# Performance work log

Measured on AMD Instinct MI355X. Metric: run time of the kernel, lower is better.

Reference implementation:

```python
import jax, jax.numpy as jnp
import numpy as np
import math

# dims
B, L, D = 2, 2048, 1024          # batch, seq len, embedding_dim
HID, ATT, H = 1024, 512, 8       # linear_hidden_dim, attention_dim, num_heads
DQK, DUV = ATT // H, HID // H    # 64, 128
NBUCK = 64                       # time_num_buckets
MAX_SPAN = 86400 * 90            # max_time_span
EPS = 1e-6
OUT_DIM = 2 * HID + 2 * ATT      # uvqk output dim = 3072


def _time_boundaries():
    # RelativeAttentionBiasModule._build_boundaries: pure log buckets
    steps = NBUCK - 1
    log_part = np.exp(np.linspace(0.0, math.log(MAX_SPAN), steps))
    b = np.unique(np.floor(np.clip(log_part, 1, None)).astype(np.int64)).astype(np.float32)
    return jnp.asarray(b)

_BOUNDARIES = _time_boundaries()  # len <= 63, indices < NBUCK


def setup_inputs() -> dict:
    key = jax.random.key(0)
    ks = jax.random.split(key, 8)
    x = jax.random.normal(ks[0], (B, L, D), dtype=jnp.float32)
    timestamps = jnp.sort(
        jax.random.randint(ks[1], (B, L), 0, 2592000), axis=-1
    )  # chronological event times (seconds)
    attn_mask = jnp.tril(jnp.ones((L, L), dtype=bool))[None].repeat(B, axis=0)  # causal
    W_uvqk = jax.random.normal(ks[2], (OUT_DIM, D), dtype=jnp.float32) * 0.02
    b_uvqk = jnp.zeros((OUT_DIM,), dtype=jnp.float32)
    time_bias = jax.random.normal(ks[3], (NBUCK, H), dtype=jnp.float32) * 0.02
    W_o = jax.random.normal(ks[4], (D, HID), dtype=jnp.float32) * 0.02
    b_o = jnp.zeros((D,), dtype=jnp.float32)
    rms_w = jnp.ones((HID,), dtype=jnp.float32)
    return {"x": x, "timestamps": timestamps, "attn_mask": attn_mask,
            "W_uvqk": W_uvqk, "b_uvqk": b_uvqk, "time_bias": time_bias,
            "W_o": W_o, "b_o": b_o, "rms_w": rms_w}


def reference(x, timestamps, attn_mask, W_uvqk, b_uvqk, time_bias, W_o, b_o, rms_w):
    Bx, Lx, _ = x.shape
    scale = 1.0 / math.sqrt(DQK)

    # fused uvqk projection + act1 (silu)
    h = jax.nn.silu(x @ W_uvqk.T + b_uvqk)  # [B, L, OUT_DIM]
    u, v, q, k = jnp.split(h, [HID, 2 * HID, 2 * HID + ATT], axis=-1)

    def heads(t, d):  # [B, L, H*d] -> [B, H, L, d]
        return t.reshape(Bx, Lx, H, d).transpose(0, 2, 1, 3)

    u = heads(u, DUV)
    v = heads(v, DUV)
    q = heads(q, DQK) * scale
    k = heads(k, DQK)

    logits = jnp.einsum('bhid,bhjd->bhij', q.astype(jnp.float32), k.astype(jnp.float32))

    # bucketized relative-time bias (per-head)
    tdiff = jnp.abs(timestamps[:, :, None] - timestamps[:, None, :])
    tdiff = jnp.clip(tdiff, 1, None).astype(jnp.float32)  # clamp_min(1)
    bk = jnp.searchsorted(_BOUNDARIES, tdiff, side='left')  # torch.bucketize right=False
    rab = time_bias[bk].transpose(0, 3, 1, 2)  # [B, H, L, L]

    # pointwise silu attention (no softmax), masked
    A = jax.nn.silu(logits + rab) * attn_mask[:, None].astype(jnp.float32)

    y = jnp.einsum('bhij,bhjd->bhid', A, v)               # [B, H, L, DUV]
    y = y.transpose(0, 2, 1, 3).reshape(Bx, Lx, HID)       # merge heads
    u_m = u.transpose(0, 2, 1, 3).reshape(Bx, Lx, HID)

    # RMSNorm then U-gate
    rms = y * jax.lax.rsqrt(jnp.mean(y * y, axis=-1, keepdims=True) + EPS) * rms_w
    y_point = rms.astype(x.dtype) * u_m

    return y_point @ W_o.T + b_o  # [B, L, D]
```

## Files before the change

kernel.cpp:

```cpp
#include <hip/hip_runtime.h>
#include <hip/hip_bf16.h>

typedef float f32x4 __attribute__((ext_vector_type(4)));
typedef short s16x8 __attribute__((ext_vector_type(8)));
typedef short s16x4 __attribute__((ext_vector_type(4)));
typedef unsigned short u16x4 __attribute__((ext_vector_type(4)));

__device__ __forceinline__ float bf2f(unsigned short u) {
    union { unsigned int i; float f; } x; x.i = ((unsigned int)u) << 16; return x.f;
}
__device__ __forceinline__ unsigned short f2bf(float f) {
    union { float f; unsigned int i; } x; x.f = f;
    unsigned int r = x.i + 0x7FFFu + ((x.i >> 16) & 1u);
    return (unsigned short)(r >> 16);
}
__device__ __forceinline__ float silu_fast(float v) {
    return v * __builtin_amdgcn_rcpf(1.f + __expf(-v));
}

#define GLDS16(gp, lp) __builtin_amdgcn_global_load_lds( \
    (const __attribute__((address_space(1))) unsigned int*)(gp), \
    (__attribute__((address_space(3))) unsigned int*)(lp), 16, 0, 0)

__global__ __launch_bounds__(256) void cvt_bucketize(
    const float* __restrict__ X, const float* __restrict__ W,
    const float* __restrict__ Wo, const int* __restrict__ TS,
    unsigned short* __restrict__ Xb, unsigned short* __restrict__ Wb,
    unsigned short* __restrict__ Wob, unsigned char* __restrict__ BK)
{
    const int tid = threadIdx.x;
    if (blockIdx.x < 8192) {
        int idx = blockIdx.x * 256 + tid;
        const float* src; unsigned short* dst; int off;
        if (idx < 1048576)       { src = X;  dst = Xb;  off = idx; }
        else if (idx < 1835008)  { src = W;  dst = Wb;  off = idx - 1048576; }
        else                     { src = Wo; dst = Wob; off = idx - 1835008; }
        f32x4 v = *reinterpret_cast<const f32x4*>(&src[(size_t)off * 4]);
        u16x4 o;
        #pragma unroll
        for (int j = 0; j < 4; ++j) o[j] = f2bf(v[j]);
        *reinterpret_cast<u16x4*>(&dst[(size_t)off * 4]) = o;
        return;
    }
    const int bid = blockIdx.x - 8192;
    const int jt = bid & 31, it = (bid >> 5) & 31, b = bid >> 10;
    if (jt > it) return;
    __shared__ int bndRaw[63];
    __shared__ int bnd[64];
    __shared__ int tsi[64], tsj[64];
    if (tid < 63) {
        double step = log(7776000.0) / 62.0;
        double v = exp(step * (double)tid);
        if (v < 1.0) v = 1.0;
        bndRaw[tid] = (int)floor(v);
    }
    if (tid >= 64 && tid < 128) tsi[tid - 64] = TS[b * 2048 + it * 64 + (tid - 64)];
    else if (tid >= 128 && tid < 192) tsj[tid - 128] = TS[b * 2048 + jt * 64 + (tid - 128)];
    __syncthreads();
    if (tid == 0) {
        int c = 0, p = -1;
        for (int i = 0; i < 63; ++i) { int x = bndRaw[i]; if (x != p) { bnd[c++] = x; p = x; } }
        for (; c < 64; ++c) bnd[c] = 0x7FFFFFFF;
    }
    __syncthreads();
    const int il = tid & 63, jc = (tid >> 6) * 16;
    const int tiv = tsi[il];
    unsigned char out[16];
    #pragma unroll
    for (int u = 0; u < 16; ++u) {
        int td = tiv - tsj[jc + u]; td = td < 0 ? -td : td; if (td < 1) td = 1;
        int pos = 0;
        #pragma unroll
        for (int st = 32; st; st >>= 1)
            if (bnd[pos + st - 1] < td) pos += st;
        out[u] = (unsigned char)pos;
    }
    *reinterpret_cast<int4*>(&BK[((size_t)b << 22) + (size_t)(it * 64 + il) * 2048 + jt * 64 + jc]) =
        *reinterpret_cast<const int4*>(out);
}

__global__ __launch_bounds__(256) void gemm_uvqk(
    const unsigned short* __restrict__ Xb, const unsigned short* __restrict__ Wb,
    const float* __restrict__ bias,
    unsigned short* __restrict__ U, unsigned short* __restrict__ Vt,
    unsigned short* __restrict__ Q, unsigned short* __restrict__ K)
{
    __shared__ __align__(16) unsigned short sA[128][64];
    __shared__ __align__(16) unsigned short sB[128][64];
    const int tid = threadIdx.x;
    const int wv = tid >> 6, lane = tid & 63;
    const int g = lane >> 4, lr = lane & 15;
    const int wid = (blockIdx.x & 7) * 96 + (blockIdx.x >> 3);
    const int m0 = (wid & 31) * 128, n0 = (wid >> 5) * 128;
    const int wr = (wv >> 1) * 64, wc = (wv & 1) * 64;
    const int ls = lr & 7;
    f32x4 acc[4][4] = {};

    for (int k0 = 0; k0 < 1024; k0 += 64) {
        #pragma unroll
        for (int c = 0; c < 4; ++c) {
            int id = c * 256 + tid;
            int row = id >> 3, c8 = id & 7;
            int sc = (c8 ^ (row & 7)) * 8;
            GLDS16(&Xb[(size_t)(m0 + row) * 1024 + k0 + sc], &sA[row][c8 * 8]);
            GLDS16(&Wb[(size_t)(n0 + row) * 1024 + k0 + sc], &sB[row][c8 * 8]);
        }
        __syncthreads();
        #pragma unroll
        for (int kq = 0; kq < 2; ++kq) {
            s16x8 afr[4], bfr[4];
            #pragma unroll
            for (int i = 0; i < 4; ++i) {
                afr[i] = *reinterpret_cast<const s16x8*>(
                    &sA[wr + i * 16 + lr][((kq * 4 + g) ^ ls) * 8]);
                bfr[i] = *reinterpret_cast<const s16x8*>(
                    &sB[wc + i * 16 + lr][((kq * 4 + g) ^ ls) * 8]);
            }
            #pragma unroll
            for (int mi = 0; mi < 4; ++mi)
                #pragma unroll
                for (int ni = 0; ni < 4; ++ni)
                    acc[mi][ni] = __builtin_amdgcn_mfma_f32_16x16x32_bf16(
                        afr[mi], bfr[ni], acc[mi][ni], 0, 0, 0);
        }
        __syncthreads();
    }

    if (n0 >= 1024 && n0 < 2048) {
        const int head = (n0 - 1024) >> 7;
        unsigned short* sT = &sA[0][0] + wv * (32 * 72);
        #pragma unroll
        for (int hh = 0; hh < 2; ++hh) {
            #pragma unroll
            for (int nn = 0; nn < 2; ++nn) {
                int ni = hh * 2 + nn;
                float bn = bias[n0 + wc + ni * 16 + lr];
                #pragma unroll
                for (int mi = 0; mi < 4; ++mi)
                    #pragma unroll
                    for (int r = 0; r < 4; ++r)
                        sT[(nn * 16 + lr) * 72 + mi * 16 + g * 4 + r] =
                            f2bf(silu_fast(acc[mi][ni][r] + bn));
            }
            #pragma unroll
            for (int c = 0; c < 4; ++c) {
                int id = c * 64 + lane;
                int row = id >> 3, ch = id & 7;
                s16x8 val = *reinterpret_cast<const s16x8*>(&sT[row * 72 + ch * 8]);
                int d = wc + hh * 32 + row;
                int mg = m0 + wr + ch * 8;
                int bb = mg >> 11, l = mg & 2047;
                *reinterpret_cast<s16x8*>(
                    &Vt[(((size_t)(bb * 8 + head) * 128 + d) << 11) + l]) = val;
            }
        }
    } else {
        #pragma unroll
        for (int ni = 0; ni < 4; ++ni) {
            int n = n0 + wc + ni * 16 + lr;
            float bn = bias[n];
            #pragma unroll
            for (int mi = 0; mi < 4; ++mi) {
                #pragma unroll
                for (int r = 0; r < 4; ++r) {
                    int m = m0 + wr + mi * 16 + g * 4 + r;
                    float v = silu_fast(acc[mi][ni][r] + bn);
                    int b = m >> 11, l = m & 2047;
                    if (n < 1024) {
                        U[(size_t)m * 1024 + n] = f2bf(v);
                    } else if (n < 2560) {
                        int dd = n - 2048, h = dd >> 6, d = dd & 63;
                        Q[((((size_t)(b * 8 + h) << 11) + l) << 6) + d] = f2bf(v * 0.125f);
                    } else {
                        int dd = n - 2560, h = dd >> 6, d = dd & 63;
                        K[((((size_t)(b * 8 + h) << 11) + l) << 6) + d] = f2bf(v);
                    }
                }
            }
        }
    }
}

__global__ __launch_bounds__(512, 1) void attn(
    const unsigned short* __restrict__ Q, const unsigned short* __restrict__ K,
    const unsigned short* __restrict__ Vt, const unsigned char* __restrict__ BK,
    const float* __restrict__ TB, unsigned short* __restrict__ Y)
{
    __shared__ __align__(16) unsigned short sK[2][2][64][64];
    __shared__ __align__(16) unsigned short sV[2][2][128][64];
    __shared__ __align__(16) unsigned char  sBK[2][2][64][64];

    const int tid = threadIdx.x, wv = tid >> 6, lane = tid & 63;
    const int g = lane >> 4, lr = lane & 15;

    const int bid = blockIdx.x;
    const int xcd = bid & 7, kix = bid >> 3;
    const int bh = 2 * xcd + (kix & 1);
    const int ti = 31 - (kix >> 1);
    const int b = bh >> 3, h = bh & 7;
    const int i0 = ti * 64;
    const int rg = wv & 3;
    const int half = wv >> 2;
    const int irow = i0 + rg * 16;
    const int P = (ti + 2) >> 1;

    const int tbl = __float_as_int(TB[lane * 8 + h]);

    const unsigned short* qb = Q + ((size_t)bh << 11) * 64;
    const unsigned short* kb = K + ((size_t)bh << 11) * 64;
    const unsigned short* vtb = Vt + ((size_t)bh << 7) * 2048;
    const unsigned char* bkb = BK + ((size_t)b << 22);

    s16x8 aq[2];
    #pragma unroll
    for (int kq = 0; kq < 2; ++kq)
        aq[kq] = *reinterpret_cast<const s16x8*>(&qb[(size_t)(irow + lr) * 64 + kq * 32 + g * 8]);

    char* sKb = (char*)&sK[0][0][0][0];
    char* sVb = (char*)&sV[0][0][0][0];
    char* sBKb = (char*)&sBK[0][0][0][0];
    const int cs = lr & 7;
    const int ib = irow + lr;

    auto stage = [&](int q, int db) {
        int jth = 2 * q + half;
        if (jth > ti) jth = 2 * q;
        const size_t j0 = (size_t)jth * 64;
        char* kd = sKb + db * 16384 + half * 8192;
        char* vd = sVb + db * 32768 + half * 16384;
        char* bkd = sBKb + db * 8192 + half * 4096;
        #pragma unroll
        for (int c = 0; c < 2; ++c) {
            int chunk = rg * 128 + c * 64 + lane;
            int row = chunk >> 3, c8 = chunk & 7;
            GLDS16(kb + (j0 + row) * 64 + ((c8 ^ (row & 7)) * 8), kd + chunk * 16);
        }
        #pragma unroll
        for (int c = 0; c < 4; ++c) {
            int chunk = rg * 256 + c * 64 + lane;
            int d = chunk >> 3, c8 = chunk & 7;
            GLDS16(vtb + (size_t)d * 2048 + j0 + ((c8 ^ (d & 7)) * 8), vd + chunk * 16);
        }
        {
            int chunk = rg * 64 + lane;
            int row = chunk >> 2, c16 = chunk & 3;
            GLDS16(bkb + (size_t)(i0 + row) * 2048 + j0 + ((c16 ^ (row & 3)) * 16), bkd + chunk * 16);
        }
    };

    f32x4 accy[8] = {};

#define COMPUTE(DB) { \
        const int jt = 2 * p + half; \
        if (jt <= ti) { \
            const char* kbase = sKb + (DB) * 16384 + half * 8192; \
            f32x4 sacc[4] = {}; \
            _Pragma("unroll") \
            for (int ni = 0; ni < 4; ++ni) { \
                _Pragma("unroll") \
                for (int kq = 0; kq < 2; ++kq) { \
                    s16x8 kf = *reinterpret_cast<const s16x8*>( \
                        kbase + (ni * 16 + lr) * 128 + (((kq * 4 + g) ^ cs) << 4)); \
                    sacc[ni] = __builtin_amdgcn_mfma_f32_16x16x32_bf16(kf, aq[kq], sacc[ni], 0, 0, 0); \
                } \
            } \
            const int j0 = jt * 64; \
            const bool diag = (jt == ti); \
            s16x4 pf[4]; \
            _Pragma("unroll") \
            for (int ni = 0; ni < 4; ++ni) { \
                unsigned int bw = *reinterpret_cast<const unsigned int*>( \
                    sBKb + (DB) * 8192 + half * 4096 + (rg * 16 + lr) * 64 + ((ni ^ (lr & 3)) << 4) + g * 4); \
                float b0 = __int_as_float(__builtin_amdgcn_ds_bpermute((int)((bw & 255u) << 2), tbl)); \
                float b1 = __int_as_float(__builtin_amdgcn_ds_bpermute((int)(((bw >> 8) & 255u) << 2), tbl)); \
                float b2 = __int_as_float(__builtin_amdgcn_ds_bpermute((int)(((bw >> 16) & 255u) << 2), tbl)); \
                float b3 = __int_as_float(__builtin_amdgcn_ds_bpermute((int)((bw >> 24) << 2), tbl)); \
                float v0 = silu_fast(sacc[ni][0] + b0); \
                float v1 = silu_fast(sacc[ni][1] + b1); \
                float v2 = silu_fast(sacc[ni][2] + b2); \
                float v3 = silu_fast(sacc[ni][3] + b3); \
                if (diag) { \
                    int jb = j0 + ni * 16 + g * 4; \
                    if (jb + 0 > ib) v0 = 0.f; \
                    if (jb + 1 > ib) v1 = 0.f; \
                    if (jb + 2 > ib) v2 = 0.f; \
                    if (jb + 3 > ib) v3 = 0.f; \
                } \
                unsigned int w0, w1; \
                asm("v_cvt_pk_bf16_f32 %0, %1, %2" : "=v"(w0) : "v"(v0), "v"(v1)); \
                asm("v_cvt_pk_bf16_f32 %0, %1, %2" : "=v"(w1) : "v"(v2), "v"(v3)); \
                union { unsigned int u_[2]; s16x4 v_; } cvt_; \
                cvt_.u_[0] = w0; cvt_.u_[1] = w1; \
                pf[ni] = cvt_.v_; \
            } \
            const char* vbase = sVb + (DB) * 32768 + half * 16384; \
            _Pragma("unroll") \
            for (int di = 0; di < 8; ++di) { \
                _Pragma("unroll") \
                for (int ni = 0; ni < 4; ++ni) { \
                    s16x4 vf = *reinterpret_cast<const s16x4*>( \
                        vbase + (di * 16 + lr) * 128 + (((2 * ni + (g >> 1)) ^ cs) << 4) + ((g & 1) << 3)); \
                    accy[di] = __builtin_amdgcn_mfma_f32_16x16x16bf16_1k(pf[ni], vf, accy[di], 0, 0, 0); \
                } \
            } \
        } }

    stage(0, 0);

    int p = 0;
    for (;;) {
        __builtin_amdgcn_s_barrier();
        if (p + 1 < P) {
            stage(p + 1, 1);
            asm volatile("s_waitcnt vmcnt(7)" ::: "memory");
        } else {
            asm volatile("s_waitcnt vmcnt(0)" ::: "memory");
        }
        __builtin_amdgcn_s_barrier();
        COMPUTE(0);
        if (++p == P) break;
        __builtin_amdgcn_s_barrier();
        if (p + 1 < P) {
            stage(p + 1, 0);
            asm volatile("s_waitcnt vmcnt(7)" ::: "memory");
        } else {
            asm volatile("s_waitcnt vmcnt(0)" ::: "memory");
        }
        __builtin_amdgcn_s_barrier();
        COMPUTE(1);
        if (++p == P) break;
    }
#undef COMPUTE

    __syncthreads();
    float* red = (float*)sVb;
    if (wv >= 4) {
        #pragma unroll
        for (int di = 0; di < 8; ++di)
            #pragma unroll
            for (int r = 0; r < 4; ++r)
                red[(rg * 16 + g * 4 + r) * 132 + di * 16 + lr] = accy[di][r];
    }
    __syncthreads();
    if (wv < 4) {
        #pragma unroll
        for (int di = 0; di < 8; ++di)
            #pragma unroll
            for (int r = 0; r < 4; ++r) {
                float s = accy[di][r] + red[(rg * 16 + g * 4 + r) * 132 + di * 16 + lr];
                Y[(size_t)((b << 11) + irow + g * 4 + r) * 1024 + h * 128 + di * 16 + lr] = f2bf(s);
            }
    }
}

__global__ __launch_bounds__(256) void rmsnorm_gate(
    const unsigned short* __restrict__ Y, const unsigned short* __restrict__ U,
    const float* __restrict__ rw, unsigned short* __restrict__ YP)
{
    __shared__ float red[4];
    const int row = blockIdx.x, tid = threadIdx.x;
    u16x4 v4 = *reinterpret_cast<const u16x4*>(&Y[(size_t)row * 1024 + tid * 4]);
    float v[4];
    #pragma unroll
    for (int j = 0; j < 4; ++j) v[j] = bf2f(v4[j]);
    float ss = v[0] * v[0] + v[1] * v[1] + v[2] * v[2] + v[3] * v[3];
    #pragma unroll
    for (int off = 32; off; off >>= 1) ss += __shfl_down(ss, off);
    if ((tid & 63) == 0) red[tid >> 6] = ss;
    __syncthreads();
    float rms = rsqrtf((red[0] + red[1] + red[2] + red[3]) * (1.f / 1024.f) + 1e-6f);
    #pragma unroll
    for (int j = 0; j < 4; ++j) {
        int c = tid * 4 + j;
        float o = v[j] * rms * rw[c] * bf2f(U[(size_t)row * 1024 + c]);
        YP[(size_t)row * 1024 + c] = f2bf(o);
    }
}

__global__ __launch_bounds__(512) void gemm_out(
    const unsigned short* __restrict__ YP, const unsigned short* __restrict__ Wob,
    const float* __restrict__ bo, float* __restrict__ OUT)
{
    __shared__ __align__(16) unsigned short sA[128][64];
    __shared__ __align__(16) unsigned short sB[128][64];
    const int tid = threadIdx.x;
    const int wv = tid >> 6, lane = tid & 63;
    const int g = lane >> 4, lr = lane & 15;
    const int wid = (blockIdx.x & 7) * 32 + (blockIdx.x >> 3);
    const int m0 = (wid & 31) * 128, n0 = (wid >> 5) * 128;
    const int wr = (wv >> 2) * 64, wc = (wv & 3) * 32;
    const int ls = lr & 7;
    f32x4 acc[4][2] = {};

    for (int k0 = 0; k0 < 1024; k0 += 64) {
        #pragma unroll
        for (int c = 0; c < 2; ++c) {
            int id = c * 512 + tid;
            int row = id >> 3, c8 = id & 7;
            int sc = (c8 ^ (row & 7)) * 8;
            GLDS16(&YP[(size_t)(m0 + row) * 1024 + k0 + sc], &sA[row][c8 * 8]);
            GLDS16(&Wob[(size_t)(n0 + row) * 1024 + k0 + sc], &sB[row][c8 * 8]);
        }
        __syncthreads();
        #pragma unroll
        for (int kq = 0; kq < 2; ++kq) {
            s16x8 afr[4], bfr[2];
            #pragma unroll
            for (int i = 0; i < 4; ++i)
                afr[i] = *reinterpret_cast<const s16x8*>(
                    &sA[wr + i * 16 + lr][((kq * 4 + g) ^ ls) * 8]);
            #pragma unroll
            for (int i = 0; i < 2; ++i)
                bfr[i] = *reinterpret_cast<const s16x8*>(
                    &sB[wc + i * 16 + lr][((kq * 4 + g) ^ ls) * 8]);
            #pragma unroll
            for (int mi = 0; mi < 4; ++mi)
                #pragma unroll
                for (int ni = 0; ni < 2; ++ni)
                    acc[mi][ni] = __builtin_amdgcn_mfma_f32_16x16x32_bf16(
                        afr[mi], bfr[ni], acc[mi][ni], 0, 0, 0);
        }
        __syncthreads();
    }

    #pragma unroll
    for (int ni = 0; ni < 2; ++ni) {
        int n = n0 + wc + ni * 16 + lr;
        float bn = bo[n];
        #pragma unroll
        for (int mi = 0; mi < 4; ++mi)
            #pragma unroll
            for (int r = 0; r < 4; ++r) {
                int m = m0 + wr + mi * 16 + g * 4 + r;
                OUT[(size_t)m * 1024 + n] = acc[mi][ni][r] + bn;
            }
    }
}

extern "C" void kernel_launch(void* const* d_in, const int* in_sizes, int n_in,
                              void* d_out, int out_size, void* d_ws, size_t ws_size,
                              hipStream_t stream) {
    const float* X     = (const float*)d_in[0];
    const int*   TS    = (const int*)d_in[1];
    const float* Wuvqk = (const float*)d_in[3];
    const float* buvqk = (const float*)d_in[4];
    const float* TB    = (const float*)d_in[5];
    const float* Wo    = (const float*)d_in[6];
    const float* bo    = (const float*)d_in[7];
    const float* rw    = (const float*)d_in[8];
    float* OUT = (float*)d_out;

    char* ws = (char*)d_ws;
    unsigned short* Qb  = (unsigned short*)(ws);
    unsigned short* Kb  = (unsigned short*)(ws + (4u << 20));
    unsigned short* Vt  = (unsigned short*)(ws + (8u << 20));
    unsigned short* Ub  = (unsigned short*)(ws + (16u << 20));
    unsigned short* Yb  = (unsigned short*)(ws + (24u << 20));
    unsigned short* Xb  = (unsigned short*)(ws + (24u << 20));
    unsigned short* Wb  = (unsigned short*)(ws + (32u << 20));
    unsigned short* YP  = (unsigned short*)(ws + (40u << 20));
    unsigned char*  BKm = (unsigned char*)(ws + (48u << 20));
    unsigned short* Wob = (unsigned short*)(ws + (56u << 20));

    cvt_bucketize<<<10240, 256, 0, stream>>>(X, Wuvqk, Wo, TS, Xb, Wb, Wob, BKm);
    gemm_uvqk<<<768, 256, 0, stream>>>(Xb, Wb, buvqk, Ub, Vt, Qb, Kb);
    attn<<<512, 512, 0, stream>>>(Qb, Kb, Vt, BKm, TB, Yb);
    rmsnorm_gate<<<4096, 256, 0, stream>>>(Yb, Ub, rw, YP);
    gemm_out<<<256, 512, 0, stream>>>(YP, Wob, bo, OUT);
}
```

Measured before the change: 144.6 us.

## Shrink attention KV tile to 32 columns and load bias bytes directly to registers

The attention kernel now stages 32-column K/V tiles per half-block instead of 64, which halves shared memory to 48KB and raises the launch-bounds occupancy hint from 1 to 6. The diagonal masking is simplified to the last iteration. Time-bucket indices are loaded from global memory straight into registers one stage ahead, instead of going through LDS. The aim is more resident blocks and less LDS traffic, at the cost of twice as many pipeline steps with their barriers and smaller MFMA batches. The raised occupancy hint may also squeeze the register budget.

Measured after the change: 174.9 us. 1.21x slower.

```diff
diff --git a/kernel.cpp b/kernel.cpp
--- a/kernel.cpp
+++ b/kernel.cpp
@@ -181,14 +181,12 @@
     }
 }
 
-__global__ __launch_bounds__(512, 1) void attn(
+__global__ __launch_bounds__(512, 6) void attn(
     const unsigned short* __restrict__ Q, const unsigned short* __restrict__ K,
     const unsigned short* __restrict__ Vt, const unsigned char* __restrict__ BK,
     const float* __restrict__ TB, unsigned short* __restrict__ Y)
 {
-    __shared__ __align__(16) unsigned short sK[2][2][64][64];
-    __shared__ __align__(16) unsigned short sV[2][2][128][64];
-    __shared__ __align__(16) unsigned char  sBK[2][2][64][64];
+    __shared__ __align__(16) char smem[49152];
 
     const int tid = threadIdx.x, wv = tid >> 6, lane = tid & 63;
     const int g = lane >> 4, lr = lane & 15;
@@ -202,138 +200,133 @@
     const int rg = wv & 3;
     const int half = wv >> 2;
     const int irow = i0 + rg * 16;
-    const int P = (ti + 2) >> 1;
+    const int P = ti + 1;
 
     const int tbl = __float_as_int(TB[lane * 8 + h]);
 
     const unsigned short* qb = Q + ((size_t)bh << 11) * 64;
     const unsigned short* kb = K + ((size_t)bh << 11) * 64;
     const unsigned short* vtb = Vt + ((size_t)bh << 7) * 2048;
-    const unsigned char* bkb = BK + ((size_t)b << 22);
+    const unsigned char* bkp = BK + ((size_t)b << 22) + (size_t)(irow + lr) * 2048 + g * 4;
 
     s16x8 aq[2];
     #pragma unroll
     for (int kq = 0; kq < 2; ++kq)
         aq[kq] = *reinterpret_cast<const s16x8*>(&qb[(size_t)(irow + lr) * 64 + kq * 32 + g * 8]);
 
-    char* sKb = (char*)&sK[0][0][0][0];
-    char* sVb = (char*)&sV[0][0][0][0];
-    char* sBKb = (char*)&sBK[0][0][0][0];
+    char* base = smem;
     const int cs = lr & 7;
     const int ib = irow + lr;
 
-    auto stage = [&](int q, int db) {
-        int jth = 2 * q + half;
-        if (jth > ti) jth = 2 * q;
-        const size_t j0 = (size_t)jth * 64;
-        char* kd = sKb + db * 16384 + half * 8192;
-        char* vd = sVb + db * 32768 + half * 16384;
-        char* bkd = sBKb + db * 8192 + half * 4096;
+    auto stage = [&](int p, int db) {
+        const int jt = 2 * p + half;
+        const size_t j0 = (size_t)jt * 32;
+        char* kd = base + db * 8192 + half * 4096;
+        char* vd = base + 16384 + db * 16384 + half * 8192;
+        {
+            int id = (rg << 6) | lane;
+            int row = id >> 3, c8 = id & 7;
+            GLDS16(kb + (j0 + row) * 64 + ((c8 ^ (row & 7)) * 8), kd + id * 16);
+        }
         #pragma unroll
         for (int c = 0; c < 2; ++c) {
-            int chunk = rg * 128 + c * 64 + lane;
-            int row = chunk >> 3, c8 = chunk & 7;
-            GLDS16(kb + (j0 + row) * 64 + ((c8 ^ (row & 7)) * 8), kd + chunk * 16);
-        }
-        #pragma unroll
-        for (int c = 0; c < 4; ++c) {
-            int chunk = rg * 256 + c * 64 + lane;
-            int d = chunk >> 3, c8 = chunk & 7;
-            GLDS16(vtb + (size_t)d * 2048 + j0 + ((c8 ^ (d & 7)) * 8), vd + chunk * 16);
-        }
-        {
-            int chunk = rg * 64 + lane;
-            int row = chunk >> 2, c16 = chunk & 3;
-            GLDS16(bkb + (size_t)(i0 + row) * 2048 + j0 + ((c16 ^ (row & 3)) * 16), bkd + chunk * 16);
+            int id = c * 256 + ((rg << 6) | lane);
+            int d = id >> 2, c16 = id & 3;
+            GLDS16(vtb + (size_t)d * 2048 + j0 + ((c16 ^ (d & 3)) * 8), vd + id * 16);
         }
     };
 
+#define BIAS_LOAD(p, bw) { const unsigned char* p_ = bkp + (size_t)(2 * (p) + half) * 32; \
+        bw[0] = *(const unsigned int*)(p_); bw[1] = *(const unsigned int*)(p_ + 16); }
+
     f32x4 accy[8] = {};
 
-#define COMPUTE(DB) { \
-        const int jt = 2 * p + half; \
-        if (jt <= ti) { \
-            const char* kbase = sKb + (DB) * 16384 + half * 8192; \
-            f32x4 sacc[4] = {}; \
+#define COMPUTE(DB, BW, p) { \
+        const int jt = 2 * (p) + half; \
+        const char* kbase = base + (DB) * 8192 + half * 4096; \
+        f32x4 sacc[2] = {}; \
+        _Pragma("unroll") \
+        for (int ni = 0; ni < 2; ++ni) { \
             _Pragma("unroll") \
-            for (int ni = 0; ni < 4; ++ni) { \
-                _Pragma("unroll") \
-                for (int kq = 0; kq < 2; ++kq) { \
-                    s16x8 kf = *reinterpret_cast<const s16x8*>( \
-                        kbase + (ni * 16 + lr) * 128 + (((kq * 4 + g) ^ cs) << 4)); \
-                    sacc[ni] = __builtin_amdgcn_mfma_f32_16x16x32_bf16(kf, aq[kq], sacc[ni], 0, 0, 0); \
-                } \
+            for (int kq = 0; kq < 2; ++kq) { \
+                s16x8 kf = *reinterpret_cast<const s16x8*>( \
+                    kbase + (ni * 16 + lr) * 128 + (((kq * 4 + g) ^ cs) << 4)); \
+                sacc[ni] = __builtin_amdgcn_mfma_f32_16x16x32_bf16(kf, aq[kq], sacc[ni], 0, 0, 0); \
             } \
-            const int j0 = jt * 64; \
-            const bool diag = (jt == ti); \
-            s16x4 pf[4]; \
+        } \
+        const int j0 = jt * 32; \
+        const bool diag = ((p) == P - 1); \
+        s16x4 pf[2]; \
+        _Pragma("unroll") \
+        for (int ni = 0; ni < 2; ++ni) { \
+            unsigned int bw = BW[ni]; \
+            float b0 = __int_as_float(__builtin_amdgcn_ds_bpermute((int)((bw & 255u) << 2), tbl)); \
+            float b1 = __int_as_float(__builtin_amdgcn_ds_bpermute((int)(((bw >> 8) & 255u) << 2), tbl)); \
+            float b2 = __int_as_float(__builtin_amdgcn_ds_bpermute((int)(((bw >> 16) & 255u) << 2), tbl)); \
+            float b3 = __int_as_float(__builtin_amdgcn_ds_bpermute((int)((bw >> 24) << 2), tbl)); \
+            float v0 = silu_fast(sacc[ni][0] + b0); \
+            float v1 = silu_fast(sacc[ni][1] + b1); \
+            float v2 = silu_fast(sacc[ni][2] + b2); \
+            float v3 = silu_fast(sacc[ni][3] + b3); \
+            if (diag) { \
+                int jb = j0 + ni * 16 + g * 4; \
+                if (jb + 0 > ib) v0 = 0.f; \
+                if (jb + 1 > ib) v1 = 0.f; \
+                if (jb + 2 > ib) v2 = 0.f; \
+                if (jb + 3 > ib) v3 = 0.f; \
+            } \
+            unsigned int w0, w1; \
+            asm("v_cvt_pk_bf16_f32 %0, %1, %2" : "=v"(w0) : "v"(v0), "v"(v1)); \
+            asm("v_cvt_pk_bf16_f32 %0, %1, %2" : "=v"(w1) : "v"(v2), "v"(v3)); \
+            union { unsigned int u_[2]; s16x4 v_; } cvt_; \
+            cvt_.u_[0] = w0; cvt_.u_[1] = w1; \
+            pf[ni] = cvt_.v_; \
+        } \
+        const char* vbase = base + 16384 + (DB) * 16384 + half * 8192; \
+        _Pragma("unroll") \
+        for (int di = 0; di < 8; ++di) { \
             _Pragma("unroll") \
-            for (int ni = 0; ni < 4; ++ni) { \
-                unsigned int bw = *reinterpret_cast<const unsigned int*>( \
-                    sBKb + (DB) * 8192 + half * 4096 + (rg * 16 + lr) * 64 + ((ni ^ (lr & 3)) << 4) + g * 4); \
-                float b0 = __int_as_float(__builtin_amdgcn_ds_bpermute((int)((bw & 255u) << 2), tbl)); \
-                float b1 = __int_as_float(__builtin_amdgcn_ds_bpermute((int)(((bw >> 8) & 255u) << 2), tbl)); \
-                float b2 = __int_as_float(__builtin_amdgcn_ds_bpermute((int)(((bw >> 16) & 255u) << 2), tbl)); \
-                float b3 = __int_as_float(__builtin_amdgcn_ds_bpermute((int)((bw >> 24) << 2), tbl)); \
-                float v0 = silu_fast(sacc[ni][0] + b0); \
-                float v1 = silu_fast(sacc[ni][1] + b1); \
-                float v2 = silu_fast(sacc[ni][2] + b2); \
-                float v3 = silu_fast(sacc[ni][3] + b3); \
-                if (diag) { \
-                    int jb = j0 + ni * 16 + g * 4; \
-                    if (jb + 0 > ib) v0 = 0.f; \
-                    if (jb + 1 > ib) v1 = 0.f; \
-                    if (jb + 2 > ib) v2 = 0.f; \
-                    if (jb + 3 > ib) v3 = 0.f; \
-                } \
-                unsigned int w0, w1; \
-                asm("v_cvt_pk_bf16_f32 %0, %1, %2" : "=v"(w0) : "v"(v0), "v"(v1)); \
-                asm("v_cvt_pk_bf16_f32 %0, %1, %2" : "=v"(w1) : "v"(v2), "v"(v3)); \
-                union { unsigned int u_[2]; s16x4 v_; } cvt_; \
-                cvt_.u_[0] = w0; cvt_.u_[1] = w1; \
-                pf[ni] = cvt_.v_; \
-            } \
-            const char* vbase = sVb + (DB) * 32768 + half * 16384; \
-            _Pragma("unroll") \
-            for (int di = 0; di < 8; ++di) { \
-                _Pragma("unroll") \
-                for (int ni = 0; ni < 4; ++ni) { \
-                    s16x4 vf = *reinterpret_cast<const s16x4*>( \
-                        vbase + (di * 16 + lr) * 128 + (((2 * ni + (g >> 1)) ^ cs) << 4) + ((g & 1) << 3)); \
-                    accy[di] = __builtin_amdgcn_mfma_f32_16x16x16bf16_1k(pf[ni], vf, accy[di], 0, 0, 0); \
-                } \
+            for (int ni = 0; ni < 2; ++ni) { \
+                s16x4 vf = *reinterpret_cast<const s16x4*>( \
+                    vbase + (di * 16 + lr) * 64 + (((ni * 2 + (g >> 1)) ^ (lr & 3)) << 4) + ((g & 1) << 3)); \
+                accy[di] = __builtin_amdgcn_mfma_f32_16x16x16bf16_1k(pf[ni], vf, accy[di], 0, 0, 0); \
             } \
         } }
 
+    unsigned int bwA[2], bwB[2];
     stage(0, 0);
+    BIAS_LOAD(0, bwA);
 
     int p = 0;
     for (;;) {
         __builtin_amdgcn_s_barrier();
         if (p + 1 < P) {
             stage(p + 1, 1);
-            asm volatile("s_waitcnt vmcnt(7)" ::: "memory");
+            BIAS_LOAD(p + 1, bwB);
+            asm volatile("s_waitcnt vmcnt(5)" ::: "memory");
         } else {
             asm volatile("s_waitcnt vmcnt(0)" ::: "memory");
         }
         __builtin_amdgcn_s_barrier();
-        COMPUTE(0);
+        COMPUTE(0, bwA, p);
         if (++p == P) break;
         __builtin_amdgcn_s_barrier();
         if (p + 1 < P) {
             stage(p + 1, 0);
-            asm volatile("s_waitcnt vmcnt(7)" ::: "memory");
+            BIAS_LOAD(p + 1, bwA);
+            asm volatile("s_waitcnt vmcnt(5)" ::: "memory");
         } else {
             asm volatile("s_waitcnt vmcnt(0)" ::: "memory");
         }
         __builtin_amdgcn_s_barrier();
-        COMPUTE(1);
+        COMPUTE(1, bwB, p);
         if (++p == P) break;
     }
 #undef COMPUTE
+#undef BIAS_LOAD
 
     __syncthreads();
-    float* red = (float*)sVb;
+    float* red = (float*)base;
     if (wv >= 4) {
         #pragma unroll
         for (int di = 0; di < 8; ++di)
```

## Enlarge uvqk GEMM tiles to 256x256 with double-buffered LDS prefetch

Applied to the files above, without the earlier changes.

Rewrites the uvqk projection GEMM to use 256x256 block tiles with 8 waves and double-buffered shared memory, splitting the prefetch of the next K-slice of A and B across the MFMA phases. It uses explicit waitcnt, s_barrier and priority hints so loads overlap the matrix work. The aim is higher data reuse per load and fewer stalls. In exchange, the grid drops to 192 blocks on a many-CU GPU, which may leave CUs idle, and register pressure rises with the larger accumulator tile.

New measurement: 133.9 us (median of 2 runs). -7.4%, faster.

```diff
diff --git a/kernel.cpp b/kernel.cpp
--- a/kernel.cpp
+++ b/kernel.cpp
@@ -79,91 +79,137 @@
         *reinterpret_cast<const int4*>(out);
 }
 
-__global__ __launch_bounds__(256) void gemm_uvqk(
+__global__ __launch_bounds__(512, 2) void gemm_uvqk(
     const unsigned short* __restrict__ Xb, const unsigned short* __restrict__ Wb,
     const float* __restrict__ bias,
     unsigned short* __restrict__ U, unsigned short* __restrict__ Vt,
     unsigned short* __restrict__ Q, unsigned short* __restrict__ K)
 {
-    __shared__ __align__(16) unsigned short sA[128][64];
-    __shared__ __align__(16) unsigned short sB[128][64];
+    __shared__ __align__(16) unsigned short smem[2][2][256][64];
     const int tid = threadIdx.x;
     const int wv = tid >> 6, lane = tid & 63;
     const int g = lane >> 4, lr = lane & 15;
-    const int wid = (blockIdx.x & 7) * 96 + (blockIdx.x >> 3);
-    const int m0 = (wid & 31) * 128, n0 = (wid >> 5) * 128;
-    const int wr = (wv >> 1) * 64, wc = (wv & 1) * 64;
+    const int wid = (blockIdx.x & 7) * 24 + (blockIdx.x >> 3);
+    const int mt = wid & 15, nt = wid >> 4;
+    const int m0 = mt * 256, n0 = nt * 256;
+    const int wm = wv >> 2, wn = wv & 3;
     const int ls = lr & 7;
-    f32x4 acc[4][4] = {};
-
-    for (int k0 = 0; k0 < 1024; k0 += 64) {
+    f32x4 acc[8][4] = {};
+
+    auto stageA = [&](int kt, int db) {
+        const int k0 = kt * 64;
         #pragma unroll
         for (int c = 0; c < 4; ++c) {
-            int id = c * 256 + tid;
+            int id = c * 512 + tid;
             int row = id >> 3, c8 = id & 7;
-            int sc = (c8 ^ (row & 7)) * 8;
-            GLDS16(&Xb[(size_t)(m0 + row) * 1024 + k0 + sc], &sA[row][c8 * 8]);
-            GLDS16(&Wb[(size_t)(n0 + row) * 1024 + k0 + sc], &sB[row][c8 * 8]);
-        }
-        __syncthreads();
-        #pragma unroll
-        for (int kq = 0; kq < 2; ++kq) {
-            s16x8 afr[4], bfr[4];
-            #pragma unroll
-            for (int i = 0; i < 4; ++i) {
-                afr[i] = *reinterpret_cast<const s16x8*>(
-                    &sA[wr + i * 16 + lr][((kq * 4 + g) ^ ls) * 8]);
-                bfr[i] = *reinterpret_cast<const s16x8*>(
-                    &sB[wc + i * 16 + lr][((kq * 4 + g) ^ ls) * 8]);
+            GLDS16(&Xb[(size_t)(m0 + row) * 1024 + k0 + (c8 ^ (row & 7)) * 8],
+                   &smem[db][0][row][c8 * 8]);
+        }
+    };
+    auto stageB = [&](int kt, int db) {
+        const int k0 = kt * 64;
+        #pragma unroll
+        for (int c = 0; c < 4; ++c) {
+            int id = c * 512 + tid;
+            int row = id >> 3, c8 = id & 7;
+            GLDS16(&Wb[(size_t)(n0 + row) * 1024 + k0 + (c8 ^ (row & 7)) * 8],
+                   &smem[db][1][row][c8 * 8]);
+        }
+    };
+
+    stageB(0, 0); stageA(0, 0);
+
+    for (int kt = 0; kt < 16; ++kt) {
+        const int db = kt & 1;
+        const unsigned short (*sA)[64] = smem[db][0];
+        const unsigned short (*sB)[64] = smem[db][1];
+        s16x8 bfr[4][2];
+        #pragma unroll
+        for (int q = 0; q < 4; ++q) {
+            if (q == 0) {
+                if (kt < 15) {
+                    stageB(kt + 1, db ^ 1);
+                    asm volatile("s_waitcnt vmcnt(4)" ::: "memory");
+                } else {
+                    asm volatile("s_waitcnt vmcnt(0)" ::: "memory");
+                }
+                __builtin_amdgcn_s_barrier();
             }
-            #pragma unroll
-            for (int mi = 0; mi < 4; ++mi)
+            s16x8 afr[2][2];
+            if (q == 0) {
                 #pragma unroll
                 for (int ni = 0; ni < 4; ++ni)
-                    acc[mi][ni] = __builtin_amdgcn_mfma_f32_16x16x32_bf16(
-                        afr[mi], bfr[ni], acc[mi][ni], 0, 0, 0);
-        }
-        __syncthreads();
-    }
+                    #pragma unroll
+                    for (int kq = 0; kq < 2; ++kq)
+                        bfr[ni][kq] = *reinterpret_cast<const s16x8*>(
+                            &sB[wn * 64 + ni * 16 + lr][((kq * 4 + g) ^ ls) * 8]);
+            }
+            #pragma unroll
+            for (int j = 0; j < 2; ++j)
+                #pragma unroll
+                for (int kq = 0; kq < 2; ++kq)
+                    afr[j][kq] = *reinterpret_cast<const s16x8*>(
+                        &sA[wm * 128 + (2 * q + j) * 16 + lr][((kq * 4 + g) ^ ls) * 8]);
+            if (q == 1 && kt < 15) stageA(kt + 1, db ^ 1);
+            asm volatile("s_waitcnt lgkmcnt(0)" ::: "memory");
+            __builtin_amdgcn_sched_barrier(0);
+            __builtin_amdgcn_s_setprio(1);
+            #pragma unroll
+            for (int kq = 0; kq < 2; ++kq)
+                #pragma unroll
+                for (int j = 0; j < 2; ++j)
+                    #pragma unroll
+                    for (int ni = 0; ni < 4; ++ni)
+                        acc[2 * q + j][ni] = __builtin_amdgcn_mfma_f32_16x16x32_bf16(
+                            afr[j][kq], bfr[ni][kq], acc[2 * q + j][ni], 0, 0, 0);
+            __builtin_amdgcn_s_setprio(0);
+            __builtin_amdgcn_s_barrier();
+        }
+    }
+    __syncthreads();
 
     if (n0 >= 1024 && n0 < 2048) {
-        const int head = (n0 - 1024) >> 7;
-        unsigned short* sT = &sA[0][0] + wv * (32 * 72);
-        #pragma unroll
-        for (int hh = 0; hh < 2; ++hh) {
-            #pragma unroll
-            for (int nn = 0; nn < 2; ++nn) {
-                int ni = hh * 2 + nn;
-                float bn = bias[n0 + wc + ni * 16 + lr];
-                #pragma unroll
-                for (int mi = 0; mi < 4; ++mi)
+        const int dglob = n0 - 1024 + wn * 64;
+        const int head = dglob >> 7, dbase = dglob & 127;
+        unsigned short* sT = &smem[0][0][0][0] + wv * 2304;
+        #pragma unroll
+        for (int mh = 0; mh < 2; ++mh) {
+            #pragma unroll
+            for (int hh = 0; hh < 2; ++hh) {
+                #pragma unroll
+                for (int nn = 0; nn < 2; ++nn) {
+                    int ni = hh * 2 + nn;
+                    float bn = bias[n0 + wn * 64 + ni * 16 + lr];
                     #pragma unroll
-                    for (int r = 0; r < 4; ++r)
-                        sT[(nn * 16 + lr) * 72 + mi * 16 + g * 4 + r] =
-                            f2bf(silu_fast(acc[mi][ni][r] + bn));
+                    for (int mi = 0; mi < 4; ++mi)
+                        #pragma unroll
+                        for (int r = 0; r < 4; ++r)
+                            sT[(nn * 16 + lr) * 72 + mi * 16 + g * 4 + r] =
+                                f2bf(silu_fast(acc[mh * 4 + mi][ni][r] + bn));
+                }
+                #pragma unroll
+                for (int c = 0; c < 4; ++c) {
+                    int id = c * 64 + lane;
+                    int row = id >> 3, ch = id & 7;
+                    s16x8 val = *reinterpret_cast<const s16x8*>(&sT[row * 72 + ch * 8]);
+                    int d = dbase + hh * 32 + row;
+                    int mg = m0 + wm * 128 + mh * 64 + ch * 8;
+                    int bb = mg >> 11, l = mg & 2047;
+                    *reinterpret_cast<s16x8*>(
+                        &Vt[(((size_t)(bb * 8 + head) * 128 + d) << 11) + l]) = val;
+                }
             }
-            #pragma unroll
-            for (int c = 0; c < 4; ++c) {
-                int id = c * 64 + lane;
-                int row = id >> 3, ch = id & 7;
-                s16x8 val = *reinterpret_cast<const s16x8*>(&sT[row * 72 + ch * 8]);
-                int d = wc + hh * 32 + row;
-                int mg = m0 + wr + ch * 8;
-                int bb = mg >> 11, l = mg & 2047;
-                *reinterpret_cast<s16x8*>(
-                    &Vt[(((size_t)(bb * 8 + head) * 128 + d) << 11) + l]) = val;
-            }
         }
     } else {
         #pragma unroll
         for (int ni = 0; ni < 4; ++ni) {
-            int n = n0 + wc + ni * 16 + lr;
+            int n = n0 + wn * 64 + ni * 16 + lr;
             float bn = bias[n];
             #pragma unroll
-            for (int mi = 0; mi < 4; ++mi) {
+            for (int mi = 0; mi < 8; ++mi) {
                 #pragma unroll
                 for (int r = 0; r < 4; ++r) {
-                    int m = m0 + wr + mi * 16 + g * 4 + r;
+                    int m = m0 + wm * 128 + mi * 16 + g * 4 + r;
                     float v = silu_fast(acc[mi][ni][r] + bn);
                     int b = m >> 11, l = m & 2047;
                     if (n < 1024) {
@@ -463,7 +509,7 @@
     unsigned short* Wob = (unsigned short*)(ws + (56u << 20));
 
     cvt_bucketize<<<10240, 256, 0, stream>>>(X, Wuvqk, Wo, TS, Xb, Wb, Wob, BKm);
-    gemm_uvqk<<<768, 256, 0, stream>>>(Xb, Wb, buvqk, Ub, Vt, Qb, Kb);
+    gemm_uvqk<<<192, 512, 0, stream>>>(Xb, Wb, buvqk, Ub, Vt, Qb, Kb);
     attn<<<512, 512, 0, stream>>>(Qb, Kb, Vt, BKm, TB, Yb);
     rmsnorm_gate<<<4096, 256, 0, stream>>>(Yb, Ub, rw, YP);
     gemm_out<<<256, 512, 0, stream>>>(YP, Wob, bo, OUT);
```
